# Kernel optimization log

Hardware: AMD Instinct MI355X
Metric: run time of the kernel (lower is better)

## Reference

```python
import jax, jax.numpy as jnp
import numpy as np

N_NODES = 100000
N_EDGES = 1600000
D_FEAT = 64  # node feature dim; apply_func indim = 2*D_FEAT, outdim = D_FEAT


def setup_inputs() -> dict:
    key = jax.random.key(0)
    k1, k2, k3, k4 = jax.random.split(key, 4)
    h = jax.random.normal(k1, (N_NODES, D_FEAT), dtype=jnp.float32)
    src = jax.random.randint(k2, (N_EDGES,), 0, N_NODES, dtype=jnp.int32)
    dst = jax.random.randint(k3, (N_EDGES,), 0, N_NODES, dtype=jnp.int32)
    W = jax.random.normal(k4, (D_FEAT, 2 * D_FEAT), dtype=jnp.float32) / jnp.sqrt(2.0 * D_FEAT)
    b = jnp.zeros((D_FEAT,), dtype=jnp.float32)
    return {"h": h, "W": W, "b": b, "src": src, "dst": dst}


def reference(h, W, b, src, dst):
    n = h.shape[0]
    # message passing: gather source features, mean-reduce per destination node
    msgs = h[src]                                                # [E, D]
    summed = jax.ops.segment_sum(msgs, dst, num_segments=n)     # [N, D]
    deg = jax.ops.segment_sum(jnp.ones(dst.shape, h.dtype), dst, num_segments=n)  # [N]
    c = summed / jnp.maximum(deg, 1.0)[:, None]                 # mean aggregate
    # update: concat(h, c) -> linear -> L2 normalize -> relu
    bundle = jnp.concatenate([h, c], axis=1) @ W.T + b           # [N, D]
    norm = jnp.linalg.norm(bundle, axis=1, keepdims=True)
    bundle = bundle / jnp.maximum(norm, 1e-12)                   # F.normalize(p=2, dim=1)
    new_h = jax.nn.relu(bundle)
    # DGL update_all only touches nodes that received messages
    h_upd = jnp.where(deg[:, None] > 0, new_h, h)
    # residual (indim == outdim)
    return h + h_upd
```

## Files before the change

### kernel.cpp

```cpp
#include <hip/hip_runtime.h>

#define DF 64
#define ELLK 32
#define BSH 9
#define WIN 128
#define CAP 32
#define OCAP 32
#define WPAD 132
#define OVL 128
#define MAXCH 800

typedef __attribute__((ext_vector_type(8))) short bf16x8;
typedef __attribute__((ext_vector_type(4))) float f32x4;

__device__ __forceinline__ unsigned short bf16rne(float f) {
    unsigned u = __float_as_uint(f);
    unsigned r = u + 0x7fffu + ((u >> 16) & 1u);
    return (unsigned short)(r >> 16);
}
__device__ __forceinline__ float b2f(unsigned short u) {
    return __uint_as_float((unsigned)u << 16);
}

__global__ __launch_bounds__(512) void conv_bin(
    const float* __restrict__ h, const float* __restrict__ W,
    const int* __restrict__ src, const int* __restrict__ dst,
    unsigned short* __restrict__ hbs, unsigned short* __restrict__ Wbs,
    unsigned* __restrict__ pairs, int* __restrict__ bcnt,
    unsigned long long* __restrict__ ovfb, int* __restrict__ bovn,
    int N, int E, int NBK, int NCH, int EPB)
{
    __shared__ unsigned hist[256];
    __shared__ int ovn_l;
    const int t = threadIdx.x, blk = blockIdx.x;
    if (t < 256) hist[t] = 0;
    if (t == 0) ovn_l = 0;
    __syncthreads();

    int tot = 1024 + (N + 1) * 8;
    for (int i = blk * 512 + t; i < tot; i += NCH * 512) {
        if (i < 1024) {
            int row = i >> 4, c8 = i & 15;
            const float* wp = &W[(size_t)row * 128 + c8 * 8];
            float4 w0 = *(const float4*)wp;
            float4 w1 = *(const float4*)(wp + 4);
            bf16x8 f;
            f[0] = (short)bf16rne(w0.x); f[1] = (short)bf16rne(w0.y);
            f[2] = (short)bf16rne(w0.z); f[3] = (short)bf16rne(w0.w);
            f[4] = (short)bf16rne(w1.x); f[5] = (short)bf16rne(w1.y);
            f[6] = (short)bf16rne(w1.z); f[7] = (short)bf16rne(w1.w);
            *(bf16x8*)&Wbs[(size_t)row * 128 + c8 * 8] = f;
        } else {
            int j = i - 1024;
            int n = j >> 3, f8 = j & 7;
            unsigned short* op = &hbs[(size_t)n * DF + f8 * 8];
            if (n == N) {
                ushort4 z = {0, 0, 0, 0};
                *(ushort4*)op = z; *(ushort4*)(op + 4) = z;
            } else {
                const float* hp = &h[(size_t)n * DF + f8 * 8];
                float4 v0 = *(const float4*)hp;
                float4 v1 = *(const float4*)(hp + 4);
                ushort4 o0, o1;
                o0.x = bf16rne(v0.x); o0.y = bf16rne(v0.y);
                o0.z = bf16rne(v0.z); o0.w = bf16rne(v0.w);
                o1.x = bf16rne(v1.x); o1.y = bf16rne(v1.y);
                o1.z = bf16rne(v1.z); o1.w = bf16rne(v1.w);
                *(ushort4*)op = o0;
                *(ushort4*)(op + 4) = o1;
            }
        }
    }

    int e0 = blk * EPB, e1 = e0 + EPB; if (e1 > E) e1 = E;
    for (int e = e0 + t; e < e1; e += 512) {
        int d = dst[e], s = src[e];
        unsigned bkt = (unsigned)d >> BSH;
        unsigned r = atomicAdd(&hist[bkt], 1u);
        if (r < CAP) {
            pairs[((size_t)bkt * NCH + blk) * CAP + r] =
                ((unsigned)(d & 511) << 17) | (unsigned)s;
        } else {
            int p = atomicAdd(&ovn_l, 1);
            if (p < OCAP)
                ovfb[(size_t)blk * OCAP + p] =
                    ((unsigned long long)(unsigned)d << 32) | (unsigned)s;
        }
    }
    __syncthreads();
    for (int i = t; i < NBK; i += 512) {
        unsigned c = hist[i];
        bcnt[(size_t)i * NCH + blk] = (int)(c < CAP ? c : CAP);
    }
    if (t == 0) bovn[blk] = (ovn_l < OCAP ? ovn_l : OCAP);
}

__global__ __launch_bounds__(512, 8) void gather_update(
    const unsigned* __restrict__ pairs, const int* __restrict__ bcnt,
    const unsigned long long* __restrict__ ovfb, const int* __restrict__ bovn,
    const unsigned short* __restrict__ hbs, const unsigned short* __restrict__ Wbs,
    const float* __restrict__ b,
    float* __restrict__ out, int N, int NBK, int NCH)
{
    __shared__ int ell_l[WIN * ELLK];
    __shared__ int cnt_l[WIN];
    __shared__ unsigned short Wl[64 * WPAD];
    __shared__ int bcnt_l[MAXCH];
    __shared__ int ovl[OVL * 2];
    __shared__ int ovn;

    const int t = threadIdx.x, lane = t & 63, wv = t >> 6;
    const int base = blockIdx.x * WIN;
    const int bk = base >> BSH;
    const int q0 = base & 511;

    for (int i = t; i < WIN; i += 512) cnt_l[i] = 0;
    if (t == 0) ovn = 0;
    for (int i = t; i < 1024; i += 512) {
        int row = i >> 4, c8 = i & 15;
        *(bf16x8*)&Wl[row * WPAD + c8 * 8] =
            *(const bf16x8*)&Wbs[(size_t)row * 128 + c8 * 8];
    }
    for (int i = t; i < NCH; i += 512)
        bcnt_l[i] = bcnt[(size_t)bk * NCH + i];
    __syncthreads();

    int nit = (NCH + 15) >> 4;
    for (int it = 0; it < nit; ++it) {
        int ch = it * 16 + wv * 2 + (lane >> 5);
        int slot = lane & 31;
        if (ch < NCH && slot < bcnt_l[ch]) {
            unsigned p = pairs[((size_t)bk * NCH + ch) * CAP + slot];
            int ld = (int)(p >> 17) - q0;
            if ((unsigned)ld < (unsigned)WIN) {
                int s = (int)(p & 131071u);
                int sl2 = atomicAdd(&cnt_l[ld], 1);
                if (sl2 < ELLK) {
                    ell_l[ld * ELLK + (((sl2 & 7) << 2) | (sl2 >> 3))] = s;
                } else {
                    int q2 = atomicAdd(&ovn, 1);
                    if (q2 < OVL) { ovl[2 * q2] = ld; ovl[2 * q2 + 1] = s; }
                }
            }
        }
    }
    for (int i = t; i < NCH; i += 512) {
        int bn = bovn[i];
        for (int j = 0; j < bn; ++j) {
            unsigned long long v = ovfb[(size_t)i * OCAP + j];
            int d = (int)(v >> 32);
            int ld = d - base;
            if ((unsigned)ld < (unsigned)WIN) {
                int s = (int)(v & 0xFFFFFFFFu);
                int sl2 = atomicAdd(&cnt_l[ld], 1);
                if (sl2 < ELLK) {
                    ell_l[ld * ELLK + (((sl2 & 7) << 2) | (sl2 >> 3))] = s;
                } else {
                    int q2 = atomicAdd(&ovn, 1);
                    if (q2 < OVL) { ovl[2 * q2] = ld; ovl[2 * q2 + 1] = s; }
                }
            }
        }
    }
    __syncthreads();

    unsigned short* csB = (unsigned short*)ell_l;
    {
        const int ew = lane >> 3;
        const int f8 = lane & 7;
        for (int i = 0; i < 16; ++i) {
            int ld = wv * 16 + i;
            int n = base + ld;
            if (n < N) {
                int cv = cnt_l[ld];
                int m = cv < ELLK ? cv : ELLK;
                int ms = __builtin_amdgcn_readfirstlane(m);
                int4 pv = ((const int4*)&ell_l[ld * ELLK])[ew];

                int i0 = (ew     < m) ? pv.x : N;
                int i1 = (ew + 8 < m) ? pv.y : N;
                bf16x8 v0 = *(const bf16x8*)&hbs[(size_t)i0 * DF + f8 * 8];
                bf16x8 v1 = *(const bf16x8*)&hbs[(size_t)i1 * DF + f8 * 8];
                bf16x8 v2 = {0,0,0,0,0,0,0,0};
                bf16x8 v3 = {0,0,0,0,0,0,0,0};
                if (ms > 16) {
                    int i2 = (ew + 16 < m) ? pv.z : N;
                    v2 = *(const bf16x8*)&hbs[(size_t)i2 * DF + f8 * 8];
                    if (ms > 24) {
                        int i3 = (ew + 24 < m) ? pv.w : N;
                        v3 = *(const bf16x8*)&hbs[(size_t)i3 * DF + f8 * 8];
                    }
                }

                float a[8];
                #pragma unroll
                for (int j = 0; j < 8; ++j)
                    a[j] = (b2f((unsigned short)v0[j]) + b2f((unsigned short)v1[j]))
                         + (b2f((unsigned short)v2[j]) + b2f((unsigned short)v3[j]));
                #pragma unroll
                for (int msk = 8; msk <= 32; msk <<= 1) {
                    #pragma unroll
                    for (int j = 0; j < 8; ++j) a[j] += __shfl_xor(a[j], msk);
                }
                if (ew == 0) {
                    bf16x8 o;
                    #pragma unroll
                    for (int j = 0; j < 8; ++j) o[j] = (short)bf16rne(a[j]);
                    int sl = f8 ^ (ld & 7);
                    *(bf16x8*)&csB[ld * 64 + sl * 8] = o;
                }
            } else if (ew == 0) {
                bf16x8 z = {0,0,0,0,0,0,0,0};
                int sl = f8 ^ (ld & 7);
                *(bf16x8*)&csB[ld * 64 + sl * 8] = z;
            }
        }
    }
    __syncthreads();

    const int c = lane & 15, q = lane >> 4;
    float bias[4];
    #pragma unroll
    for (int nt = 0; nt < 4; ++nt) bias[nt] = b[nt * 16 + c];

    int ovnc = ovn; if (ovnc > OVL) ovnc = OVL;

    int wn0 = wv * 16;
    int nm = base + wn0 + c;
    int nmc = nm < N ? nm : N - 1;
    int dtot = cnt_l[wn0 + c];
    float inv = 1.0f / fmaxf((float)dtot, 1.0f);

    bf16x8 a0 = *(const bf16x8*)&hbs[(size_t)nmc * DF + q * 8];
    bf16x8 a1 = *(const bf16x8*)&hbs[(size_t)nmc * DF + 32 + q * 8];
    bf16x8 a2, a3;
    #pragma unroll
    for (int kc = 0; kc < 2; ++kc) {
        int srow = wn0 + c;
        int sl = (kc * 4 + q) ^ (srow & 7);
        bf16x8 u = *(const bf16x8*)&csB[srow * 64 + sl * 8];
        float e[8];
        #pragma unroll
        for (int i = 0; i < 8; ++i) e[i] = b2f((unsigned short)u[i]);
        if (ovnc > 0) {
            for (int t2 = 0; t2 < ovnc; ++t2) {
                if (ovl[2 * t2] == wn0 + c) {
                    bf16x8 hu = *(const bf16x8*)&hbs[(size_t)ovl[2 * t2 + 1] * DF + kc * 32 + q * 8];
                    #pragma unroll
                    for (int i = 0; i < 8; ++i) e[i] += b2f((unsigned short)hu[i]);
                }
            }
        }
        bf16x8 f;
        #pragma unroll
        for (int i = 0; i < 8; ++i) f[i] = (short)bf16rne(e[i] * inv);
        if (kc == 0) a2 = f; else a3 = f;
    }

    #define WF(nt, kt) (*(const bf16x8*)&Wl[((nt) * 16 + c) * WPAD + (kt) * 32 + q * 8])
    f32x4 acc0 = {bias[0], bias[0], bias[0], bias[0]};
    f32x4 acc1 = {bias[1], bias[1], bias[1], bias[1]};
    f32x4 acc2 = {bias[2], bias[2], bias[2], bias[2]};
    f32x4 acc3 = {bias[3], bias[3], bias[3], bias[3]};
    acc0 = __builtin_amdgcn_mfma_f32_16x16x32_bf16(a0, WF(0,0), acc0, 0, 0, 0);
    acc0 = __builtin_amdgcn_mfma_f32_16x16x32_bf16(a1, WF(0,1), acc0, 0, 0, 0);
    acc0 = __builtin_amdgcn_mfma_f32_16x16x32_bf16(a2, WF(0,2), acc0, 0, 0, 0);
    acc0 = __builtin_amdgcn_mfma_f32_16x16x32_bf16(a3, WF(0,3), acc0, 0, 0, 0);
    acc1 = __builtin_amdgcn_mfma_f32_16x16x32_bf16(a0, WF(1,0), acc1, 0, 0, 0);
    acc1 = __builtin_amdgcn_mfma_f32_16x16x32_bf16(a1, WF(1,1), acc1, 0, 0, 0);
    acc1 = __builtin_amdgcn_mfma_f32_16x16x32_bf16(a2, WF(1,2), acc1, 0, 0, 0);
    acc1 = __builtin_amdgcn_mfma_f32_16x16x32_bf16(a3, WF(1,3), acc1, 0, 0, 0);
    acc2 = __builtin_amdgcn_mfma_f32_16x16x32_bf16(a0, WF(2,0), acc2, 0, 0, 0);
    acc2 = __builtin_amdgcn_mfma_f32_16x16x32_bf16(a1, WF(2,1), acc2, 0, 0, 0);
    acc2 = __builtin_amdgcn_mfma_f32_16x16x32_bf16(a2, WF(2,2), acc2, 0, 0, 0);
    acc2 = __builtin_amdgcn_mfma_f32_16x16x32_bf16(a3, WF(2,3), acc2, 0, 0, 0);
    acc3 = __builtin_amdgcn_mfma_f32_16x16x32_bf16(a0, WF(3,0), acc3, 0, 0, 0);
    acc3 = __builtin_amdgcn_mfma_f32_16x16x32_bf16(a1, WF(3,1), acc3, 0, 0, 0);
    acc3 = __builtin_amdgcn_mfma_f32_16x16x32_bf16(a2, WF(3,2), acc3, 0, 0, 0);
    acc3 = __builtin_amdgcn_mfma_f32_16x16x32_bf16(a3, WF(3,3), acc3, 0, 0, 0);
    #undef WF

    float ss[4];
    #pragma unroll
    for (int r = 0; r < 4; ++r)
        ss[r] = acc0[r] * acc0[r] + acc1[r] * acc1[r]
              + acc2[r] * acc2[r] + acc3[r] * acc3[r];
    #pragma unroll
    for (int msk = 1; msk <= 8; msk <<= 1) {
        ss[0] += __shfl_xor(ss[0], msk);
        ss[1] += __shfl_xor(ss[1], msk);
        ss[2] += __shfl_xor(ss[2], msk);
        ss[3] += __shfl_xor(ss[3], msk);
    }
    #pragma unroll
    for (int r = 0; r < 4; ++r) {
        int nr = base + wn0 + q * 4 + r;
        int dr = __shfl(dtot, q * 4 + r);
        if (nr < N) {
            float rin = 1.0f / fmaxf(sqrtf(ss[r]), 1e-12f);
            const unsigned short* hp = &hbs[(size_t)nr * DF + c];
            float hv0 = b2f(hp[0]),  hv1 = b2f(hp[16]);
            float hv2 = b2f(hp[32]), hv3 = b2f(hp[48]);
            bool up = dr > 0;
            float o0 = hv0 + (up ? fmaxf(acc0[r] * rin, 0.f) : hv0);
            float o1 = hv1 + (up ? fmaxf(acc1[r] * rin, 0.f) : hv1);
            float o2 = hv2 + (up ? fmaxf(acc2[r] * rin, 0.f) : hv2);
            float o3 = hv3 + (up ? fmaxf(acc3[r] * rin, 0.f) : hv3);
            float* op = &out[(size_t)nr * DF + c];
            op[0] = o0; op[16] = o1; op[32] = o2; op[48] = o3;
        }
    }
}

extern "C" void kernel_launch(void* const* d_in, const int* in_sizes, int n_in,
                              void* d_out, int out_size, void* d_ws, size_t ws_size,
                              hipStream_t stream) {
    const float* h   = (const float*)d_in[0];
    const float* W   = (const float*)d_in[1];
    const float* b   = (const float*)d_in[2];
    const int*   src = (const int*)d_in[3];
    const int*   dst = (const int*)d_in[4];
    float* out = (float*)d_out;

    const int N = in_sizes[0] / DF;
    const int E = in_sizes[3];
    const int NBK = (N + 511) >> BSH;
    int NCH = (E + 2047) / 2048;
    if (NCH > MAXCH) NCH = MAXCH;
    const int EPB = (E + NCH - 1) / NCH;

    unsigned short* Wbs = (unsigned short*)d_ws;
    unsigned short* hbs = Wbs + 64 * 128;
    unsigned* pairs = (unsigned*)(hbs + (((size_t)(N + 1) * DF + 15) & ~(size_t)15));
    int* bcnt = (int*)(pairs + (size_t)NBK * NCH * CAP);
    int* bovn = bcnt + (((size_t)NBK * NCH + 15) & ~(size_t)15);
    unsigned long long* ovfb =
        (unsigned long long*)(bovn + ((NCH + 15) & ~15));

    conv_bin<<<NCH, 512, 0, stream>>>(
        h, W, src, dst, hbs, Wbs, pairs, bcnt, ovfb, bovn, N, E, NBK, NCH, EPB);

    gather_update<<<(N + WIN - 1) / WIN, 512, 0, stream>>>(
        pairs, bcnt, ovfb, bovn, hbs, Wbs, b, out, N, NBK, NCH);
}
```

Measured before the change: 172.8 us.

## Fuse binning and gather-update kernels into one persistent kernel with grid barrier

Merges the conv_bin and gather_update kernels into a single launch separated by a software grid barrier built on an atomic counter. The chunk count is now tied to the node-window count, so each block bins one edge chunk and then handles one node window. This removes a kernel launch and the drain between the two kernels, at the cost of a hipMemsetAsync for the barrier counter. The barrier can deadlock unless all 782 blocks are co-resident on the GPU, and the binning chunk size also changes.

```diff
diff --git a/kernel.cpp b/kernel.cpp
--- a/kernel.cpp
+++ b/kernel.cpp
@@ -22,19 +22,41 @@
     return __uint_as_float((unsigned)u << 16);
 }
 
-__global__ __launch_bounds__(512) void conv_bin(
+__device__ __forceinline__ void grid_barrier(int* bar, int nblk) {
+    __syncthreads();
+    if (threadIdx.x == 0) {
+        __threadfence();
+        int v = atomicAdd(bar, 1);
+        int target = (v / nblk + 1) * nblk;
+        while (atomicAdd(bar, 0) < target)
+            __builtin_amdgcn_s_sleep(8);
+        __threadfence();
+    }
+    __syncthreads();
+}
+
+__global__ __launch_bounds__(512, 8) void sage_all(
     const float* __restrict__ h, const float* __restrict__ W,
-    const int* __restrict__ src, const int* __restrict__ dst,
-    unsigned short* __restrict__ hbs, unsigned short* __restrict__ Wbs,
-    unsigned* __restrict__ pairs, int* __restrict__ bcnt,
-    unsigned long long* __restrict__ ovfb, int* __restrict__ bovn,
-    int N, int E, int NBK, int NCH, int EPB)
+    const float* __restrict__ b, const int* __restrict__ src,
+    const int* __restrict__ dst, unsigned short* __restrict__ hbs,
+    unsigned short* __restrict__ Wbs, unsigned* __restrict__ pairs,
+    int* __restrict__ bcnt, unsigned long long* __restrict__ ovfb,
+    int* __restrict__ bovn, int* __restrict__ bar,
+    float* __restrict__ out, int N, int E, int NBK, int NCH, int EPB)
 {
-    __shared__ unsigned hist[256];
-    __shared__ int ovn_l;
-    const int t = threadIdx.x, blk = blockIdx.x;
-    if (t < 256) hist[t] = 0;
-    if (t == 0) ovn_l = 0;
+    __shared__ int ell_l[WIN * ELLK];
+    __shared__ int cnt_l[WIN];
+    __shared__ unsigned short Wl[64 * WPAD];
+    __shared__ int bcnt_l[MAXCH];
+    __shared__ int ovl[OVL * 2];
+    __shared__ int ovn;
+
+    const int t = threadIdx.x, lane = t & 63, wv = t >> 6;
+    const int blk = blockIdx.x;
+
+    unsigned* hist = (unsigned*)ell_l;
+    for (int i = t; i < 256; i += 512) hist[i] = 0;
+    if (t == 0) ovn = 0;
     __syncthreads();
 
     int tot = 1024 + (N + 1) * 8;
@@ -81,7 +103,7 @@
             pairs[((size_t)bkt * NCH + blk) * CAP + r] =
                 ((unsigned)(d & 511) << 17) | (unsigned)s;
         } else {
-            int p = atomicAdd(&ovn_l, 1);
+            int p = atomicAdd(&ovn, 1);
             if (p < OCAP)
                 ovfb[(size_t)blk * OCAP + p] =
                     ((unsigned long long)(unsigned)d << 32) | (unsigned)s;
@@ -92,30 +114,16 @@
         unsigned c = hist[i];
         bcnt[(size_t)i * NCH + blk] = (int)(c < CAP ? c : CAP);
     }
-    if (t == 0) bovn[blk] = (ovn_l < OCAP ? ovn_l : OCAP);
-}
-
-__global__ __launch_bounds__(512, 8) void gather_update(
-    const unsigned* __restrict__ pairs, const int* __restrict__ bcnt,
-    const unsigned long long* __restrict__ ovfb, const int* __restrict__ bovn,
-    const unsigned short* __restrict__ hbs, const unsigned short* __restrict__ Wbs,
-    const float* __restrict__ b,
-    float* __restrict__ out, int N, int NBK, int NCH)
-{
-    __shared__ int ell_l[WIN * ELLK];
-    __shared__ int cnt_l[WIN];
-    __shared__ unsigned short Wl[64 * WPAD];
-    __shared__ int bcnt_l[MAXCH];
-    __shared__ int ovl[OVL * 2];
-    __shared__ int ovn;
-
-    const int t = threadIdx.x, lane = t & 63, wv = t >> 6;
-    const int base = blockIdx.x * WIN;
+    if (t == 0) bovn[blk] = (ovn < OCAP ? ovn : OCAP);
+
+    grid_barrier(bar, NCH);
+
+    const int base = blk * WIN;
     const int bk = base >> BSH;
     const int q0 = base & 511;
 
+    if (t == 0) ovn = 0;
     for (int i = t; i < WIN; i += 512) cnt_l[i] = 0;
-    if (t == 0) ovn = 0;
     for (int i = t; i < 1024; i += 512) {
         int row = i >> 4, c8 = i & 15;
         *(bf16x8*)&Wl[row * WPAD + c8 * 8] =
@@ -322,12 +330,11 @@
     const int*   dst = (const int*)d_in[4];
     float* out = (float*)d_out;
 
-    const int N = in_sizes[0] / DF;
-    const int E = in_sizes[3];
-    const int NBK = (N + 511) >> BSH;
-    int NCH = (E + 2047) / 2048;
-    if (NCH > MAXCH) NCH = MAXCH;
-    const int EPB = (E + NCH - 1) / NCH;
+    int N = in_sizes[0] / DF;
+    int E = in_sizes[3];
+    int NBK = (N + 511) >> BSH;
+    int NCH = (N + WIN - 1) / WIN;
+    int EPB = (E + NCH - 1) / NCH;
 
     unsigned short* Wbs = (unsigned short*)d_ws;
     unsigned short* hbs = Wbs + 64 * 128;
@@ -336,10 +343,11 @@
     int* bovn = bcnt + (((size_t)NBK * NCH + 15) & ~(size_t)15);
     unsigned long long* ovfb =
         (unsigned long long*)(bovn + ((NCH + 15) & ~15));
-
-    conv_bin<<<NCH, 512, 0, stream>>>(
-        h, W, src, dst, hbs, Wbs, pairs, bcnt, ovfb, bovn, N, E, NBK, NCH, EPB);
-
-    gather_update<<<(N + WIN - 1) / WIN, 512, 0, stream>>>(
-        pairs, bcnt, ovfb, bovn, hbs, Wbs, b, out, N, NBK, NCH);
-}
+    int* bar = (int*)(ovfb + (size_t)NCH * OCAP);
+
+    hipMemsetAsync(bar, 0, sizeof(int), stream);
+
+    sage_all<<<NCH, 512, 0, stream>>>(
+        h, W, b, src, dst, hbs, Wbs, pairs, bcnt, ovfb, bovn, bar,
+        out, N, E, NBK, NCH, EPB);
+}
```

After: 270.4 us. 56.5% more time.
